# Kernel tuning notes

Measured on AMD Instinct MI355X. Metric: run time of the kernel, lower is better.

Reference implementation:

```python
import jax, jax.numpy as jnp
import numpy as np

# dims: B graphs, NE entity nodes, NR relation nodes, N total nodes, D=hsz, H heads, P prop steps
B, NE, NR, D, H, P = 4, 1536, 512, 128, 4, 2
N = NE + NR
DH = D // H
RV = 500  # relation vocab
EPS = 1e-5


def setup_inputs() -> dict:
    key = jax.random.key(0)
    ks = jax.random.split(key, 20)
    s = 0.02
    inp = {
        "vents": jax.random.normal(ks[0], (B, NE, D), dtype=jnp.float32),
        "rels": jax.random.randint(ks[1], (B, NR), 0, RV),
        "adj": jax.random.randint(ks[2], (B, N, N), 0, 2, dtype=jnp.int32),
        "entlens": jnp.full((B,), NE, dtype=jnp.int32),
        "renc_w": jax.random.normal(ks[3], (RV, D), dtype=jnp.float32) * s,
        # per-prop-step attention params (torch Linear stored as [in, out])
        "Wq": jax.random.normal(ks[4], (P, D, D)) * s,
        "bq": jnp.zeros((P, D)),
        "Wk": jax.random.normal(ks[5], (P, D, D)) * s,
        "bk": jnp.zeros((P, D)),
        "Wv": jax.random.normal(ks[6], (P, D, D)) * s,
        "bv": jnp.zeros((P, D)),
        "Wo": jax.random.normal(ks[7], (P, D, D)) * s,
        "bo": jnp.zeros((P, D)),
        # Block FFN hsz -> 4*hsz -> hsz
        "l1_w": jax.random.normal(ks[8], (P, D, 4 * D)) * s,
        "l1_b": jnp.zeros((P, 4 * D)),
        "l2_w": jax.random.normal(ks[9], (P, 4 * D, D)) * s,
        "l2_b": jnp.zeros((P, D)),
        # ln_1 is used for BOTH norms in Block (faithful to original bug)
        "ln_g": jnp.ones((P, D)),
        "ln_b": jnp.zeros((P, D)),
        # PReLU per-channel slope, torch default 0.25
        "prelu_a": jnp.full((P, 4 * D), 0.25, dtype=jnp.float32),
    }
    return inp


def _ln(x, g, b):
    m = x.mean(-1, keepdims=True)
    v = ((x - m) ** 2).mean(-1, keepdims=True)
    return (x - m) / jnp.sqrt(v + EPS) * g + b


def reference(vents, rels, adj, entlens, renc_w,
              Wq, bq, Wk, bk, Wv, bv, Wo, bo,
              l1_w, l1_b, l2_w, l2_b, ln_g, ln_b, prelu_a):
    # vgraph_i = cat(vents[i][:entlens[i]], renc(rels[i])) -> all graphs same size, batched
    vgraph = jnp.concatenate([vents, renc_w[rels]], axis=1)  # [B, N, D]
    mask = (adj == 0)  # [B, N, N] True = masked out
    scale = 1.0 / np.sqrt(DH).astype(np.float32)
    for p in range(P):
        q_in = vgraph
        kv_in = jax.lax.stop_gradient(vgraph)  # dense path: ngraph is detached
        Q = (q_in @ Wq[p] + bq[p]).reshape(B, N, H, DH)
        K = (kv_in @ Wk[p] + bk[p]).reshape(B, N, H, DH)
        V = (kv_in @ Wv[p] + bv[p]).reshape(B, N, H, DH)
        scores = jnp.einsum('bihd,bjhd->bhij', Q, K) * scale  # [B, H, N, N]
        scores = jnp.where(mask[:, None, :, :], -1e9, scores)
        A = jax.nn.softmax(scores, axis=-1)
        O = jnp.einsum('bhij,bjhd->bihd', A, V).reshape(B, N, D) @ Wo[p] + bo[p]
        # Block feed-forward (dropout = identity in eval)
        t = _ln(O, ln_g[p], ln_b[p])
        h1 = t @ l1_w[p] + l1_b[p]
        h1 = jnp.where(h1 >= 0, h1, prelu_a[p] * h1)  # PReLU
        q2 = h1 @ l2_w[p] + l2_b[p]
        vgraph = _ln(q2 + t, ln_g[p], ln_b[p])
    glob = vgraph[jnp.arange(B), entlens]  # vgraph[entlens[i]] per graph -> [B, D]
    gents = vgraph  # all graphs same length, no padding needed -> [B, N, D]
    emask = jnp.ones((B, N), dtype=bool)  # arange(N) <= N is all True
    return glob, gents, emask
```

## Files before the change

kernel.cpp:

```cpp
#include <hip/hip_runtime.h>
#include <hip/hip_bf16.h>

typedef __bf16 bf16;
typedef __bf16 bf16x4 __attribute__((ext_vector_type(4)));
typedef __bf16 bf16x8 __attribute__((ext_vector_type(8)));
typedef float f32x4 __attribute__((ext_vector_type(4)));
typedef float f32x16 __attribute__((ext_vector_type(16)));

#define B_ 4
#define NE_ 1536
#define NR_ 512
#define N_ 2048
#define D_ 128
#define H_ 4
#define DH_ 32
#define P_ 2
#define M_ (B_*N_)
#define NW_ (N_/32)
#define SK_ 4
#define KCH_ (N_/SK_)
#define NIT_ (KCH_/64)

__device__ __forceinline__ f32x4 mfma16(bf16x8 a, bf16x8 b, f32x4 c) {
    return __builtin_amdgcn_mfma_f32_16x16x32_bf16(a, b, c, 0, 0, 0);
}
__device__ __forceinline__ f32x16 mfma32(bf16x8 a, bf16x8 b, f32x16 c) {
    return __builtin_amdgcn_mfma_f32_32x32x16_bf16(a, b, c, 0, 0, 0);
}
__device__ __forceinline__ unsigned cvtpk(float lo, float hi) {
    unsigned r;
    asm("v_cvt_pk_bf16_f32 %0, %1, %2" : "=v"(r) : "v"(lo), "v"(hi));
    return r;
}
__device__ __forceinline__ void swap32(unsigned& a, unsigned& b) {
    asm("v_permlane32_swap_b32 %0, %1" : "+v"(a), "+v"(b));
}
__device__ __forceinline__ void gload16(const void* g, void* l) {
    __builtin_amdgcn_global_load_lds(
        (const __attribute__((address_space(1))) void*)g,
        (__attribute__((address_space(3))) void*)l, 16, 0, 0);
}

#define VGN_ (B_*N_*D_)
#define MKN_ (B_*N_*NW_)
#define PPER_ (3*16384 + 16384 + 65536 + 65536 + 384)
#define PRN_ (P_*PPER_)
__global__ void k_prep(const float* __restrict__ vents, const int* __restrict__ rels,
                       const float* __restrict__ renc, const int* __restrict__ adj,
                       const float* __restrict__ Wq, const float* __restrict__ Wk,
                       const float* __restrict__ Wv, const float* __restrict__ Wo,
                       const float* __restrict__ l1w, const float* __restrict__ l2w,
                       const float* __restrict__ bq, const float* __restrict__ bk,
                       const float* __restrict__ bv,
                       bf16* __restrict__ vb, unsigned int* __restrict__ mw,
                       bf16* __restrict__ wqkvT, float* __restrict__ bqkv,
                       bf16* __restrict__ woT, bf16* __restrict__ l1T,
                       bf16* __restrict__ l2T) {
    const float SC = 0.25503330560513437f;
    int idx = blockIdx.x * 256 + threadIdx.x;
    if (idx < VGN_) {
        int d = idx & (D_ - 1);
        int n = (idx >> 7) & (N_ - 1);
        int b = idx >> 18;
        float v;
        if (n < NE_) v = vents[((size_t)(b * NE_ + n)) * D_ + d];
        else         v = renc[(size_t)rels[b * NR_ + (n - NE_)] * D_ + d];
        vb[idx] = (bf16)v;
        return;
    }
    idx -= VGN_;
    if (idx < MKN_) {
        const int4* a = (const int4*)(adj + (size_t)idx * 32);
        unsigned int w = 0;
#pragma unroll
        for (int q = 0; q < 8; ++q) {
            int4 t = a[q];
            w |= (t.x != 0 ? 1u : 0u) << (q * 4 + 0);
            w |= (t.y != 0 ? 1u : 0u) << (q * 4 + 1);
            w |= (t.z != 0 ? 1u : 0u) << (q * 4 + 2);
            w |= (t.w != 0 ? 1u : 0u) << (q * 4 + 3);
        }
        mw[idx] = w;
        return;
    }
    idx -= MKN_;
    if (idx >= PRN_) return;
    int p = idx / PPER_;
    int r = idx % PPER_;
    if (r < 3 * 16384) {
        int which = r / 16384, e = r % 16384;
        int o = e >> 7, i = e & 127;
        const float* W = which == 0 ? Wq : (which == 1 ? Wk : Wv);
        float v = W[(size_t)(p * 128 + i) * 128 + o];
        if (which == 0) v *= SC;
        wqkvT[(size_t)(p * 384 + which * 128 + o) * 128 + i] = (bf16)v;
    } else if ((r -= 3 * 16384) < 16384) {
        int o = r >> 7, i = r & 127;
        woT[(size_t)(p * 128 + o) * 128 + i] = (bf16)Wo[(size_t)(p * 128 + i) * 128 + o];
    } else if ((r -= 16384) < 65536) {
        int o = r >> 7, i = r & 127;
        l1T[(size_t)(p * 512 + o) * 128 + i] = (bf16)l1w[(size_t)(p * 128 + i) * 512 + o];
    } else if ((r -= 65536) < 65536) {
        int o = r >> 9, i = r & 511;
        l2T[(size_t)(p * 128 + o) * 512 + i] = (bf16)l2w[(size_t)(p * 512 + i) * 128 + o];
    } else {
        r -= 65536;
        float v = r < 128 ? bq[p * 128 + r] * SC
                          : (r < 256 ? bk[p * 128 + r - 128] : bv[p * 128 + r - 256]);
        bqkv[p * 384 + r] = v;
    }
}

__global__ __launch_bounds__(256) void k_qkv(
        const bf16* __restrict__ X, const bf16* __restrict__ WT,
        const float* __restrict__ bias,
        bf16* __restrict__ Qout, bf16* __restrict__ Kout,
        bf16* __restrict__ VTout) {
    int lane = threadIdx.x & 63, wid = threadIdx.x >> 6;
    int wr = wid >> 1, wc = wid & 1;
    int m0 = blockIdx.x * 64 + wr * 32;
    int n0 = blockIdx.y * 64 + wc * 32;
    int lr = lane & 15, lg = lane >> 4;
    f32x4 acc[2][2];
#pragma unroll
    for (int mi = 0; mi < 2; ++mi)
#pragma unroll
        for (int ni = 0; ni < 2; ++ni)
            acc[mi][ni] = f32x4{0.f, 0.f, 0.f, 0.f};

    for (int k0 = 0; k0 < 128; k0 += 32) {
        bf16x8 a[2], bb[2];
#pragma unroll
        for (int mi = 0; mi < 2; ++mi)
            a[mi] = *(const bf16x8*)(X + (size_t)(m0 + mi * 16 + lr) * 128 + k0 + lg * 8);
#pragma unroll
        for (int ni = 0; ni < 2; ++ni)
            bb[ni] = *(const bf16x8*)(WT + (size_t)(n0 + ni * 16 + lr) * 128 + k0 + lg * 8);
#pragma unroll
        for (int mi = 0; mi < 2; ++mi)
#pragma unroll
            for (int ni = 0; ni < 2; ++ni)
                acc[mi][ni] = mfma16(a[mi], bb[ni], acc[mi][ni]);
    }
#pragma unroll
    for (int mi = 0; mi < 2; ++mi) {
#pragma unroll
        for (int ni = 0; ni < 2; ++ni) {
            int col = n0 + ni * 16 + lr;
            float bs = bias[col];
            int rowb = m0 + mi * 16 + lg * 4;
            if (col < 128) {
#pragma unroll
                for (int r = 0; r < 4; ++r)
                    Qout[(size_t)(rowb + r) * D_ + col] = (bf16)(acc[mi][ni][r] + bs);
            } else if (col < 256) {
#pragma unroll
                for (int r = 0; r < 4; ++r)
                    Kout[(size_t)(rowb + r) * D_ + (col - 128)] = (bf16)(acc[mi][ni][r] + bs);
            } else {
                int d = col - 256, h = d >> 5, dh = d & 31;
                int b = rowb >> 11, nn = rowb & (N_ - 1);
                bf16x4 pk;
#pragma unroll
                for (int r = 0; r < 4; ++r) pk[r] = (bf16)(acc[mi][ni][r] + bs);
                *(bf16x4*)(VTout + ((size_t)(b * H_ + h) * DH_ + dh) * N_ + nn) = pk;
            }
        }
    }
}

__global__ __launch_bounds__(256) void k_attn(
    const bf16* __restrict__ Q, const bf16* __restrict__ Kt,
    const bf16* __restrict__ VT, const unsigned int* __restrict__ mw,
    bf16* __restrict__ partO, float* __restrict__ partML) {
    __shared__ __align__(16) char kbuf[4][4096];
    __shared__ __align__(16) char vbuf[4][4096];
    int wid = threadIdx.x >> 6;
    int lane = threadIdx.x & 63;
    int ql = lane & 31, hf = lane >> 5;
    int bh = blockIdx.y;
    int b = bh >> 2, h = bh & 3;
    int kc = blockIdx.z;
    int qg = blockIdx.x * 128 + wid * 32 + ql;
    const size_t bnD = (size_t)b * N_ * D_;

    const bf16* qp = Q + bnD + (size_t)qg * D_ + h * 32 + hf * 8;
    bf16x8 qf0 = *(const bf16x8*)(qp);
    bf16x8 qf1 = *(const bf16x8*)(qp + 16);

    const uint4* mp4 = (const uint4*)(mw + ((size_t)b * N_ + qg) * NW_ + kc * (KCH_ / 32));
    uint4 mk0 = mp4[0], mk1 = mp4[1], mk2 = mp4[2], mk3 = mp4[3];
    unsigned mword[16] = {mk0.x, mk0.y, mk0.z, mk0.w, mk1.x, mk1.y, mk1.z, mk1.w,
                          mk2.x, mk2.y, mk2.z, mk2.w, mk3.x, mk3.y, mk3.z, mk3.w};

    const char* kg = (const char*)(Kt + bnD + (size_t)(kc * KCH_) * D_) + h * 64;
    const char* vg = (const char*)(VT + (size_t)(bh * DH_) * N_ + kc * KCH_);

    f32x16 of;
#pragma unroll
    for (int i = 0; i < 16; ++i) of[i] = 0.f;
    const f32x16 zero16 = of;
    float lsum = 0.f;

#define STAGE(bufi, it) do {                                                   \
        int k0s = (it) * 64;                                                   \
        gload16(kg + (size_t)(k0s + lane) * 256 + wid * 16,                    \
                kbuf[bufi] + wid * 1024);                                      \
        gload16(vg + ((size_t)(lane & 31) * N_ + k0s) * 2 +                    \
                    (2 * wid + (lane >> 5)) * 16,                              \
                vbuf[bufi] + wid * 1024);                                      \
    } while (0)

    STAGE(0, 0);
    STAGE(1, 1);

#pragma unroll
    for (int it = 0; it < NIT_; ++it) {
        int cur = it & 3;
        if (it + 2 < NIT_) STAGE((it + 2) & 3, it + 2);
        if (it < NIT_ - 2)       asm volatile("s_waitcnt vmcnt(4)" ::: "memory");
        else if (it == NIT_ - 2) asm volatile("s_waitcnt vmcnt(2)" ::: "memory");
        else                     asm volatile("s_waitcnt vmcnt(0)" ::: "memory");
        __builtin_amdgcn_s_barrier();
        __builtin_amdgcn_sched_barrier(0);

#pragma unroll
        for (int kb = 0; kb < 2; ++kb) {
            bf16x8 kf0 = *(const bf16x8*)(kbuf[cur] + hf * 1024 + (kb * 32 + ql) * 16);
            bf16x8 kf1 = *(const bf16x8*)(kbuf[cur] + 2048 + hf * 1024 + (kb * 32 + ql) * 16);
            f32x16 s = mfma32(kf0, qf0, zero16);
            s = mfma32(kf1, qf1, s);

            unsigned wsh = mword[it * 2 + kb] >> (hf * 4);
            float p[16];
#pragma unroll
            for (int r = 0; r < 16; ++r) {
                int bitp = (r & 3) + 8 * (r >> 2);
                float e = __builtin_amdgcn_exp2f(s[r]);
                p[r] = ((wsh >> bitp) & 1u) ? e : 0.f;
            }
            float a0 = (p[0] + p[1]) + (p[2] + p[3]);
            float a1 = (p[4] + p[5]) + (p[6] + p[7]);
            float a2 = (p[8] + p[9]) + (p[10] + p[11]);
            float a3 = (p[12] + p[13]) + (p[14] + p[15]);
            lsum += (a0 + a1) + (a2 + a3);

            unsigned lo0 = cvtpk(p[0], p[1]),   hi0 = cvtpk(p[2], p[3]);
            unsigned lo1 = cvtpk(p[4], p[5]),   hi1 = cvtpk(p[6], p[7]);
            unsigned lo2 = cvtpk(p[8], p[9]),   hi2 = cvtpk(p[10], p[11]);
            unsigned lo3 = cvtpk(p[12], p[13]), hi3 = cvtpk(p[14], p[15]);
            swap32(lo0, lo1); swap32(hi0, hi1);
            swap32(lo2, lo3); swap32(hi2, hi3);
            union { unsigned u[4]; bf16x8 v; } f0, f1;
            f0.u[0] = lo0; f0.u[1] = hi0; f0.u[2] = lo1; f0.u[3] = hi1;
            f1.u[0] = lo2; f1.u[1] = hi2; f1.u[2] = lo3; f1.u[3] = hi3;

            bf16x8 va = *(const bf16x8*)(vbuf[cur] + ((kb * 2 + 0) * 2 + hf) * 512 + ql * 16);
            bf16x8 vb2 = *(const bf16x8*)(vbuf[cur] + ((kb * 2 + 1) * 2 + hf) * 512 + ql * 16);
            __builtin_amdgcn_s_setprio(1);
            of = mfma32(va, f0.v, of);
            of = mfma32(vb2, f1.v, of);
            __builtin_amdgcn_s_setprio(0);
        }
    }
#undef STAGE

    lsum += __shfl_xor(lsum, 32, 64);
    size_t pb = ((size_t)(kc * 16 + bh) * N_ + qg) * 32;
#pragma unroll
    for (int g = 0; g < 4; ++g) {
        union { unsigned u[2]; bf16x4 v; } pk;
        pk.u[0] = cvtpk(of[4 * g + 0], of[4 * g + 1]);
        pk.u[1] = cvtpk(of[4 * g + 2], of[4 * g + 3]);
        *(bf16x4*)(partO + pb + 8 * g + 4 * hf) = pk.v;
    }
    if (lane < 32)
        partML[(size_t)(kc * 16 + bh) * N_ + qg] = lsum;
}

template <bool LAST>
__global__ __launch_bounds__(512) void k_ffn(
        const bf16* __restrict__ partO, const float* __restrict__ partML,
        const bf16* __restrict__ woT, const float* __restrict__ bo,
        const bf16* __restrict__ l1T, const float* __restrict__ l1b,
        const float* __restrict__ pra,
        const bf16* __restrict__ l2T, const float* __restrict__ l2b,
        const float* __restrict__ lng, const float* __restrict__ lnb,
        const int* __restrict__ entl, float* __restrict__ gout,
        bf16* __restrict__ vbout) {
    __shared__ __align__(16) char Obuf[16 * 256];
    __shared__ __align__(16) char Tbuf[16 * 256];
    __shared__ __align__(16) char Hbuf[16 * 1024];
    __shared__ float lst[8][16][2];
    int t = threadIdx.x;
    int lane = t & 63, wid = t >> 6;
    int lr = lane & 15, lg = lane >> 4;
    int m0 = blockIdx.x * 16;

    {
        int i = t >> 5, u = t & 31;
        int r = m0 + i, b = r >> 11, q = r & (N_ - 1);
        int h = u >> 3, dh4 = u & 7;
        int bh = b * 4 + h;
        float L = 0.f;
        f32x4 o = {0.f, 0.f, 0.f, 0.f};
#pragma unroll
        for (int kc = 0; kc < SK_; ++kc) {
            size_t base = (size_t)(kc * 16 + bh) * N_ + q;
            L += partML[base];
            bf16x4 pv = *(const bf16x4*)(partO + base * 32 + dh4 * 4);
#pragma unroll
            for (int j = 0; j < 4; ++j) o[j] += (float)pv[j];
        }
        float rL = 1.f / L;
        bf16x4 pk;
#pragma unroll
        for (int j = 0; j < 4; ++j) pk[j] = (bf16)(o[j] * rL);
        *(bf16x4*)(Obuf + i * 256 + ((u * 8) ^ ((i & 7) << 4))) = pk;
    }
    __syncthreads();

    float tvx[4];
    {
        int n0 = wid * 16;
        f32x4 acc = {0.f, 0.f, 0.f, 0.f};
#pragma unroll
        for (int k0 = 0; k0 < 128; k0 += 32) {
            bf16x8 a = *(const bf16x8*)(Obuf + lr * 256 + (((k0 + lg * 8) * 2) ^ ((lr & 7) << 4)));
            bf16x8 bb = *(const bf16x8*)(woT + (size_t)(n0 + lr) * 128 + k0 + lg * 8);
            acc = mfma16(a, bb, acc);
        }
        int col = n0 + lr;
        float bs = bo[col];
#pragma unroll
        for (int r2 = 0; r2 < 4; ++r2) tvx[r2] = acc[r2] + bs;
#pragma unroll
        for (int r2 = 0; r2 < 4; ++r2) {
            float sv = tvx[r2], qv = tvx[r2] * tvx[r2];
#pragma unroll
            for (int msk = 1; msk < 16; msk <<= 1) {
                sv += __shfl_xor(sv, msk, 64);
                qv += __shfl_xor(qv, msk, 64);
            }
            if (lr == 0) { lst[wid][lg * 4 + r2][0] = sv; lst[wid][lg * 4 + r2][1] = qv; }
        }
        __syncthreads();
#pragma unroll
        for (int r2 = 0; r2 < 4; ++r2) {
            int row = lg * 4 + r2;
            float S = 0.f, Q2 = 0.f;
#pragma unroll
            for (int w2 = 0; w2 < 8; ++w2) { S += lst[w2][row][0]; Q2 += lst[w2][row][1]; }
            float mean = S * (1.f / 128.f);
            float var = Q2 * (1.f / 128.f) - mean * mean;
            float rstd = rsqrtf(var + 1e-5f);
            float o = (tvx[r2] - mean) * rstd * lng[col] + lnb[col];
            tvx[r2] = o;
            *(bf16*)(Tbuf + row * 256 + ((col * 2) ^ ((row & 7) << 4))) = (bf16)o;
        }
    }
    __syncthreads();

    {
        int n0 = wid * 64;
        f32x4 acc[4];
#pragma unroll
        for (int ni = 0; ni < 4; ++ni) acc[ni] = f32x4{0.f, 0.f, 0.f, 0.f};
#pragma unroll
        for (int k0 = 0; k0 < 128; k0 += 32) {
            bf16x8 a = *(const bf16x8*)(Tbuf + lr * 256 + (((k0 + lg * 8) * 2) ^ ((lr & 7) << 4)));
#pragma unroll
            for (int ni = 0; ni < 4; ++ni) {
                bf16x8 bb = *(const bf16x8*)(l1T + (size_t)(n0 + ni * 16 + lr) * 128 + k0 + lg * 8);
                acc[ni] = mfma16(a, bb, acc[ni]);
            }
        }
#pragma unroll
        for (int ni = 0; ni < 4; ++ni) {
            int col = n0 + ni * 16 + lr;
            float bs = l1b[col], sl = pra[col];
#pragma unroll
            for (int r2 = 0; r2 < 4; ++r2) {
                int row = lg * 4 + r2;
                float v = acc[ni][r2] + bs;
                v = v >= 0.f ? v : sl * v;
                *(bf16*)(Hbuf + row * 1024 + ((col * 2) ^ ((row & 7) << 4))) = (bf16)v;
            }
        }
    }
    __syncthreads();

    {
        int n0 = wid * 16;
        f32x4 acc = {0.f, 0.f, 0.f, 0.f};
#pragma unroll
        for (int k0 = 0; k0 < 512; k0 += 32) {
            bf16x8 a = *(const bf16x8*)(Hbuf + lr * 1024 + (((k0 + lg * 8) * 2) ^ ((lr & 7) << 4)));
            bf16x8 bb = *(const bf16x8*)(l2T + (size_t)(n0 + lr) * 512 + k0 + lg * 8);
            acc = mfma16(a, bb, acc);
        }
        int col = n0 + lr;
        float bs = l2b[col];
        float vx[4];
#pragma unroll
        for (int r2 = 0; r2 < 4; ++r2)
            vx[r2] = acc[r2] + bs + tvx[r2];
        __syncthreads();
#pragma unroll
        for (int r2 = 0; r2 < 4; ++r2) {
            float sv = vx[r2], qv = vx[r2] * vx[r2];
#pragma unroll
            for (int msk = 1; msk < 16; msk <<= 1) {
                sv += __shfl_xor(sv, msk, 64);
                qv += __shfl_xor(qv, msk, 64);
            }
            if (lr == 0) { lst[wid][lg * 4 + r2][0] = sv; lst[wid][lg * 4 + r2][1] = qv; }
        }
        __syncthreads();
#pragma unroll
        for (int r2 = 0; r2 < 4; ++r2) {
            int row = lg * 4 + r2;
            float S = 0.f, Q2 = 0.f;
#pragma unroll
            for (int w2 = 0; w2 < 8; ++w2) { S += lst[w2][row][0]; Q2 += lst[w2][row][1]; }
            float mean = S * (1.f / 128.f);
            float var = Q2 * (1.f / 128.f) - mean * mean;
            float rstd = rsqrtf(var + 1e-5f);
            float o = (vx[r2] - mean) * rstd * lng[col] + lnb[col];
            size_t rowg = (size_t)(m0 + row);
            vbout[rowg * 128 + col] = (bf16)o;
            if (LAST) {
                float* gents = gout + 512;
                gents[rowg * 128 + col] = o;
                int b = (int)(rowg >> 11);
                if ((int)(rowg & (N_ - 1)) == entl[b])
                    gout[b * 128 + col] = o;
            }
        }
        if (LAST && t < 16) {
            gout[512 + (size_t)M_ * 128 + m0 + t] = 1.0f;
        }
    }
}

extern "C" void kernel_launch(void* const* d_in, const int* in_sizes, int n_in,
                              void* d_out, int out_size, void* d_ws, size_t ws_size,
                              hipStream_t stream) {
    const float* vents = (const float*)d_in[0];
    const int*   rels  = (const int*)d_in[1];
    const int*   adj   = (const int*)d_in[2];
    const int*   entl  = (const int*)d_in[3];
    const float* renc  = (const float*)d_in[4];
    const float* Wq = (const float*)d_in[5];
    const float* bq = (const float*)d_in[6];
    const float* Wk = (const float*)d_in[7];
    const float* bk = (const float*)d_in[8];
    const float* Wv = (const float*)d_in[9];
    const float* bv = (const float*)d_in[10];
    const float* Wo = (const float*)d_in[11];
    const float* bo = (const float*)d_in[12];
    const float* l1w = (const float*)d_in[13];
    const float* l1b = (const float*)d_in[14];
    const float* l2w = (const float*)d_in[15];
    const float* l2b = (const float*)d_in[16];
    const float* lng = (const float*)d_in[17];
    const float* lnb = (const float*)d_in[18];
    const float* pra = (const float*)d_in[19];

    char* w = (char*)d_ws;
    auto alloc = [&](size_t bytes) { char* r = w; w += (bytes + 255) & ~(size_t)255; return r; };
    bf16*  vb    = (bf16*)alloc((size_t)M_ * D_ * 2);
    unsigned int* mw = (unsigned int*)alloc((size_t)B_ * N_ * NW_ * 4);
    bf16*  wqkvT = (bf16*)alloc((size_t)P_ * 384 * 128 * 2);
    float* bqkv  = (float*)alloc((size_t)P_ * 384 * 4);
    bf16*  woT   = (bf16*)alloc((size_t)P_ * 128 * 128 * 2);
    bf16*  l1T   = (bf16*)alloc((size_t)P_ * 512 * 128 * 2);
    bf16*  l2T   = (bf16*)alloc((size_t)P_ * 128 * 512 * 2);
    bf16*  Qb    = (bf16*)alloc((size_t)M_ * D_ * 2);
    bf16*  Kb    = (bf16*)alloc((size_t)M_ * D_ * 2);
    bf16*  VTb   = (bf16*)alloc((size_t)M_ * D_ * 2);
    bf16*  partO  = (bf16*)alloc((size_t)SK_ * 16 * N_ * 32 * 2);
    float* partML = (float*)alloc((size_t)SK_ * 16 * N_ * 4);
    float* gout  = (float*)d_out;

    const int PRTOT = VGN_ + MKN_ + PRN_;
    k_prep<<<(PRTOT + 255) / 256, 256, 0, stream>>>(
        vents, rels, renc, adj, Wq, Wk, Wv, Wo, l1w, l2w, bq, bk, bv,
        vb, mw, wqkvT, bqkv, woT, l1T, l2T);
    for (int p = 0; p < P_; ++p) {
        k_qkv<<<dim3(M_ / 64, 384 / 64), 256, 0, stream>>>(
            vb, wqkvT + (size_t)p * 384 * 128, bqkv + p * 384, Qb, Kb, VTb);
        k_attn<<<dim3(N_ / 128, B_ * H_, SK_), 256, 0, stream>>>(Qb, Kb, VTb, mw, partO, partML);
        if (p == P_ - 1)
            k_ffn<true><<<M_ / 16, 512, 0, stream>>>(
                partO, partML, woT + (size_t)p * 128 * 128, bo + p * 128,
                l1T + (size_t)p * 512 * 128, l1b + p * 512, pra + p * 512,
                l2T + (size_t)p * 128 * 512, l2b + p * 128,
                lng + p * 128, lnb + p * 128, entl, gout, vb);
        else
            k_ffn<false><<<M_ / 16, 512, 0, stream>>>(
                partO, partML, woT + (size_t)p * 128 * 128, bo + p * 128,
                l1T + (size_t)p * 512 * 128, l1b + p * 512, pra + p * 512,
                l2T + (size_t)p * 128 * 512, l2b + p * 128,
                lng + p * 128, lnb + p * 128, entl, nullptr, vb);
    }
}
```

Before: 131.1 us.

## Fuse next-step QKV projection into FFN epilogue and remap attention block order

The first FFN kernel now keeps its layer-normed output in shared memory and computes the next propagation step's Q, K and V projection there, writing them directly. This removes the second QKV launch and the bf16 round-trip of the node features through global memory. The attention kernel also remaps its flat block index so that consecutive blocks land on different XCD-style groups, which changes how K/V chunks share cache. The cost is extra work and register pressure in the FFN kernel, and uncoalesced scalar Q/K stores.

```diff
diff --git a/kernel.cpp b/kernel.cpp
--- a/kernel.cpp
+++ b/kernel.cpp
@@ -178,10 +178,13 @@
     int wid = threadIdx.x >> 6;
     int lane = threadIdx.x & 63;
     int ql = lane & 31, hf = lane >> 5;
-    int bh = blockIdx.y;
+    int hw = blockIdx.x + 16 * blockIdx.y + 256 * blockIdx.z;
+    int work = (hw & 7) * 128 + (hw >> 3);
+    int qx = work & 15;
+    int bh = (work >> 4) & 15;
+    int kc = work >> 8;
     int b = bh >> 2, h = bh & 3;
-    int kc = blockIdx.z;
-    int qg = blockIdx.x * 128 + wid * 32 + ql;
+    int qg = qx * 128 + wid * 32 + ql;
     const size_t bnD = (size_t)b * N_ * D_;
 
     const bf16* qp = Q + bnD + (size_t)qg * D_ + h * 32 + hf * 8;
@@ -286,8 +289,10 @@
         const float* __restrict__ pra,
         const bf16* __restrict__ l2T, const float* __restrict__ l2b,
         const float* __restrict__ lng, const float* __restrict__ lnb,
+        const bf16* __restrict__ wqkvT2, const float* __restrict__ bqkv2,
         const int* __restrict__ entl, float* __restrict__ gout,
-        bf16* __restrict__ vbout) {
+        bf16* __restrict__ Qout, bf16* __restrict__ Kout,
+        bf16* __restrict__ VTout) {
     __shared__ __align__(16) char Obuf[16 * 256];
     __shared__ __align__(16) char Tbuf[16 * 256];
     __shared__ __align__(16) char Hbuf[16 * 1024];
@@ -428,17 +433,56 @@
             float rstd = rsqrtf(var + 1e-5f);
             float o = (vx[r2] - mean) * rstd * lng[col] + lnb[col];
             size_t rowg = (size_t)(m0 + row);
-            vbout[rowg * 128 + col] = (bf16)o;
             if (LAST) {
                 float* gents = gout + 512;
                 gents[rowg * 128 + col] = o;
                 int b = (int)(rowg >> 11);
                 if ((int)(rowg & (N_ - 1)) == entl[b])
                     gout[b * 128 + col] = o;
-            }
-        }
-        if (LAST && t < 16) {
+            } else {
+                *(bf16*)(Obuf + row * 256 + ((col * 2) ^ ((row & 7) << 4))) = (bf16)o;
+            }
+        }
+        if (LAST && t < 16)
             gout[512 + (size_t)M_ * 128 + m0 + t] = 1.0f;
+    }
+
+    if (!LAST) {
+        __syncthreads();
+        int n0q = wid * 48;
+        f32x4 acc[3];
+#pragma unroll
+        for (int ni = 0; ni < 3; ++ni) acc[ni] = f32x4{0.f, 0.f, 0.f, 0.f};
+#pragma unroll
+        for (int k0 = 0; k0 < 128; k0 += 32) {
+            bf16x8 a = *(const bf16x8*)(Obuf + lr * 256 + (((k0 + lg * 8) * 2) ^ ((lr & 7) << 4)));
+#pragma unroll
+            for (int ni = 0; ni < 3; ++ni) {
+                bf16x8 bb = *(const bf16x8*)(wqkvT2 + (size_t)(n0q + ni * 16 + lr) * 128 + k0 + lg * 8);
+                acc[ni] = mfma16(a, bb, acc[ni]);
+            }
+        }
+#pragma unroll
+        for (int ni = 0; ni < 3; ++ni) {
+            int col = n0q + ni * 16 + lr;
+            float bs = bqkv2[col];
+            int rowb = m0 + lg * 4;
+            if (col < 128) {
+#pragma unroll
+                for (int r = 0; r < 4; ++r)
+                    Qout[(size_t)(rowb + r) * D_ + col] = (bf16)(acc[ni][r] + bs);
+            } else if (col < 256) {
+#pragma unroll
+                for (int r = 0; r < 4; ++r)
+                    Kout[(size_t)(rowb + r) * D_ + (col - 128)] = (bf16)(acc[ni][r] + bs);
+            } else {
+                int d = col - 256, h = d >> 5, dh = d & 31;
+                int b = rowb >> 11, nn = rowb & (N_ - 1);
+                bf16x4 pk;
+#pragma unroll
+                for (int r = 0; r < 4; ++r) pk[r] = (bf16)(acc[ni][r] + bs);
+                *(bf16x4*)(VTout + ((size_t)(b * H_ + h) * DH_ + dh) * N_ + nn) = pk;
+            }
         }
     }
 }
@@ -487,21 +531,16 @@
     k_prep<<<(PRTOT + 255) / 256, 256, 0, stream>>>(
         vents, rels, renc, adj, Wq, Wk, Wv, Wo, l1w, l2w, bq, bk, bv,
         vb, mw, wqkvT, bqkv, woT, l1T, l2T);
-    for (int p = 0; p < P_; ++p) {
-        k_qkv<<<dim3(M_ / 64, 384 / 64), 256, 0, stream>>>(
-            vb, wqkvT + (size_t)p * 384 * 128, bqkv + p * 384, Qb, Kb, VTb);
-        k_attn<<<dim3(N_ / 128, B_ * H_, SK_), 256, 0, stream>>>(Qb, Kb, VTb, mw, partO, partML);
-        if (p == P_ - 1)
-            k_ffn<true><<<M_ / 16, 512, 0, stream>>>(
-                partO, partML, woT + (size_t)p * 128 * 128, bo + p * 128,
-                l1T + (size_t)p * 512 * 128, l1b + p * 512, pra + p * 512,
-                l2T + (size_t)p * 128 * 512, l2b + p * 128,
-                lng + p * 128, lnb + p * 128, entl, gout, vb);
-        else
-            k_ffn<false><<<M_ / 16, 512, 0, stream>>>(
-                partO, partML, woT + (size_t)p * 128 * 128, bo + p * 128,
-                l1T + (size_t)p * 512 * 128, l1b + p * 512, pra + p * 512,
-                l2T + (size_t)p * 128 * 512, l2b + p * 128,
-                lng + p * 128, lnb + p * 128, entl, nullptr, vb);
-    }
-}
+    k_qkv<<<dim3(M_ / 64, 384 / 64), 256, 0, stream>>>(
+        vb, wqkvT, bqkv, Qb, Kb, VTb);
+    k_attn<<<dim3(16, 16, SK_), 256, 0, stream>>>(Qb, Kb, VTb, mw, partO, partML);
+    k_ffn<false><<<M_ / 16, 512, 0, stream>>>(
+        partO, partML, woT, bo, l1T, l1b, pra, l2T, l2b, lng, lnb,
+        wqkvT + (size_t)384 * 128, bqkv + 384, entl, nullptr, Qb, Kb, VTb);
+    k_attn<<<dim3(16, 16, SK_), 256, 0, stream>>>(Qb, Kb, VTb, mw, partO, partML);
+    k_ffn<true><<<M_ / 16, 512, 0, stream>>>(
+        partO, partML, woT + (size_t)128 * 128, bo + 128,
+        l1T + (size_t)512 * 128, l1b + 512, pra + 512,
+        l2T + (size_t)128 * 512, l2b + 128, lng + 128, lnb + 128,
+        wqkvT, bqkv, entl, gout, Qb, Kb, VTb);
+}
```

After: 131.8 us. No clear change (+0.5%).
